# Kernel optimization log

Measured on AMD Instinct MI355X. Metric: run time of the kernel, lower is better.

The kernel has to match this reference:

```python
import jax, jax.numpy as jnp
import numpy as np

N, E, IN, H, OUT = 100000, 1200000, 128, 64, 2
L = 3          # num GCN layers
EPS = 1e-5     # BatchNorm eps


def setup_inputs() -> dict:
    key = jax.random.key(0)
    ks = jax.random.split(key, 14)
    x = jax.random.normal(ks[0], (N, IN), dtype=jnp.float32)
    edge_index = jax.random.randint(ks[1], (2, E), 0, N, dtype=jnp.int64)
    # GCNConv weights (glorot-ish scale) and biases
    w0 = jax.random.normal(ks[2], (IN, H), dtype=jnp.float32) / np.float32(np.sqrt(IN))
    w1 = jax.random.normal(ks[3], (H, H), dtype=jnp.float32) / np.float32(np.sqrt(H))
    w2 = jax.random.normal(ks[4], (H, H), dtype=jnp.float32) / np.float32(np.sqrt(H))
    biases = jax.random.normal(ks[5], (L, H), dtype=jnp.float32) * 0.01
    # BatchNorm (eval mode): gamma, beta, running mean/var per layer
    gamma = jnp.ones((L, H), jnp.float32) + 0.1 * jax.random.normal(ks[6], (L, H), dtype=jnp.float32)
    beta = 0.1 * jax.random.normal(ks[7], (L, H), dtype=jnp.float32)
    run_mean = 0.1 * jax.random.normal(ks[8], (L, H), dtype=jnp.float32)
    run_var = 0.5 + jax.random.uniform(ks[9], (L, H), dtype=jnp.float32)  # strictly positive
    # classifier
    cls_w = jax.random.normal(ks[10], (H, OUT), dtype=jnp.float32) / np.float32(np.sqrt(H))
    cls_b = jnp.zeros((OUT,), jnp.float32)
    return {"x": x, "edge_index": edge_index, "w0": w0, "w1": w1, "w2": w2,
            "biases": biases, "gamma": gamma, "beta": beta,
            "run_mean": run_mean, "run_var": run_var,
            "cls_w": cls_w, "cls_b": cls_b}


def reference(x, edge_index, w0, w1, w2, biases, gamma, beta, run_mean, run_var, cls_w, cls_b):
    n = x.shape[0]
    loop = jnp.arange(n, dtype=edge_index.dtype)
    row = jnp.concatenate([edge_index[0], loop])  # source (with self-loops)
    col = jnp.concatenate([edge_index[1], loop])  # target (with self-loops)
    # symmetric normalization: D^{-1/2} (A+I) D^{-1/2}, degree on target index
    deg = jax.ops.segment_sum(jnp.ones(row.shape, x.dtype), col, num_segments=n)
    dinv = jnp.where(deg > 0, jax.lax.rsqrt(deg), 0.0)
    norm = dinv[row] * dinv[col]  # [E+N]

    h = x
    for l, w in enumerate((w0, w1, w2)):
        h = h @ w                                                   # [N,H]
        msg = norm[:, None] * h[row]                                # gather + scale [E+N,H]
        h = jax.ops.segment_sum(msg, col, num_segments=n) + biases[l]
        # BatchNorm1d (eval) + ReLU
        scale = gamma[l] * jax.lax.rsqrt(run_var[l] + EPS)
        h = jax.nn.relu((h - run_mean[l]) * scale + beta[l])
        # dropout is identity in eval mode
    return h @ cls_w + cls_b  # [N, OUT]
```

## Files before the change

kernel.cpp:

```cpp
#include <hip/hip_runtime.h>
#include <hip/hip_fp16.h>

#define EPS 1e-5f
#define ABITS 9
#define ACHUNK 4096
#define BCAP 8192
#define BCSR 12288
#define CSHIFT 13
#define NCHUNK 16

typedef _Float16 half8 __attribute__((ext_vector_type(8)));
typedef float floatx4 __attribute__((ext_vector_type(4)));


__global__ __launch_bounds__(256) void bucketA_kernel(const int* __restrict__ ei, int E,
                                                      int* __restrict__ bucket_fill, unsigned* __restrict__ tmp) {
    __shared__ int2 edg[ACHUNK];
    __shared__ int hist[256], lbase[256], lcur[256];
    int t = threadIdx.x;
    hist[t] = 0; lcur[t] = 0;
    __syncthreads();
    int e0 = blockIdx.x * ACHUNK;
    int e1 = e0 + ACHUNK; if (e1 > E) e1 = E;
    int ne = e1 - e0;
    for (int idx = t; idx < ne; idx += 256) {
        int r = ei[e0 + idx], c = ei[E + e0 + idx];
        edg[idx] = make_int2(r, c);
        atomicAdd(&hist[c >> ABITS], 1);
    }
    __syncthreads();
    int h = hist[t];
    if (h) lbase[t] = atomicAdd(&bucket_fill[t], h);
    __syncthreads();
    for (int idx = t; idx < ne; idx += 256) {
        int2 e = edg[idx];
        int b = e.y >> ABITS;
        int l = atomicAdd(&lcur[b], 1);
        tmp[(size_t)b * BCAP + lbase[b] + l] = ((unsigned)(e.y & 511) << 17) | (unsigned)e.x;
    }
}

__global__ __launch_bounds__(256) void bucketB_kernel(const unsigned* __restrict__ tmp,
                                                      const int* __restrict__ bucket_fill,
                                                      int2* __restrict__ rowse, float* __restrict__ dinv,
                                                      int* __restrict__ csr, int* __restrict__ perm, int n) {
    __shared__ unsigned edg[BCAP];
    __shared__ int cnt2[512 * NCHUNK];
    __shared__ int ps[256];
    __shared__ int ccnt[16], cbaseS[16];
    int b = blockIdx.x, t = threadIdx.x;
    int n0 = b << ABITS;
    int cntN = n - n0; if (cntN > 512) cntN = 512;
    int ne = bucket_fill[b]; if (ne > BCAP) ne = BCAP;
    int base = b * BCAP;
    int cbase = b * BCSR;
    if (t < 16) ccnt[t] = 0;
    for (int i = t; i < 512 * NCHUNK; i += 256) cnt2[i] = 0;
    for (int idx = t; idx < ne; idx += 256) edg[idx] = tmp[(size_t)base + idx];
    __syncthreads();
    for (int idx = t; idx < ne; idx += 256) {
        unsigned e = edg[idx];
        int dstOff = e >> 17, src = e & 0x1FFFF;
        atomicAdd(&cnt2[dstOff * NCHUNK + (src >> CSHIFT)], 1);
    }
    __syncthreads();
    int c0 = 0, c1 = 0;
#pragma unroll
    for (int c = 0; c < NCHUNK; ++c) {
        c0 += cnt2[(2 * t) * NCHUNK + c];
        c1 += cnt2[(2 * t + 1) * NCHUNK + c];
    }
    int k0c = (c0 + 7) >> 3; if (k0c > 15) k0c = 15;
    int k1c = (c1 + 7) >> 3; if (k1c > 15) k1c = 15;
    int rank0 = 0, rank1 = 0;
    if (2 * t < cntN)     rank0 = atomicAdd(&ccnt[k0c], 1);
    if (2 * t + 1 < cntN) rank1 = atomicAdd(&ccnt[k1c], 1);
    int p0 = (c0 + 7) & ~7, p1 = (c1 + 7) & ~7;
    int s = p0 + p1;
    ps[t] = s;
    __syncthreads();
    for (int off = 1; off < 256; off <<= 1) {
        int u = (t >= off) ? ps[t - off] : 0;
        __syncthreads();
        ps[t] += u;
        __syncthreads();
    }
    int excl = ps[t] - s;
    int st0 = cbase + excl, st1 = cbase + excl + p0;
    if (2 * t < cntN) {
        rowse[n0 + 2 * t] = make_int2(st0, st0 + c0);
        dinv[n0 + 2 * t] = rsqrtf((float)(c0 + 1));
    }
    if (2 * t + 1 < cntN) {
        rowse[n0 + 2 * t + 1] = make_int2(st1, st1 + c1);
        dinv[n0 + 2 * t + 1] = rsqrtf((float)(c1 + 1));
    }
    if (2 * t < cntN)
        for (int j = c0; j < p0; ++j) csr[st0 + j] = n0 + 2 * t;
    if (2 * t + 1 < cntN)
        for (int j = c1; j < p1; ++j) csr[st1 + j] = n0 + 2 * t + 1;
    int run = st0;
#pragma unroll
    for (int c = 0; c < NCHUNK; ++c) {
        int v = cnt2[(2 * t) * NCHUNK + c];
        cnt2[(2 * t) * NCHUNK + c] = run;
        run += v;
    }
    run = st1;
#pragma unroll
    for (int c = 0; c < NCHUNK; ++c) {
        int v = cnt2[(2 * t + 1) * NCHUNK + c];
        cnt2[(2 * t + 1) * NCHUNK + c] = run;
        run += v;
    }
    if (t < 16) {
        int sacc = 0;
        for (int j = 0; j < t; ++j) sacc += ccnt[j];
        cbaseS[t] = sacc;
    }
    __syncthreads();
    if (2 * t < cntN)     perm[n0 + cbaseS[k0c] + rank0] = n0 + 2 * t;
    if (2 * t + 1 < cntN) perm[n0 + cbaseS[k1c] + rank1] = n0 + 2 * t + 1;
    for (int idx = t; idx < ne; idx += 256) {
        unsigned e = edg[idx];
        int dstOff = e >> 17, src = e & 0x1FFFF;
        int key = dstOff * NCHUNK + (src >> CSHIFT);
        int pos = atomicAdd(&cnt2[key], 1);
        csr[pos] = src;
    }
}


template <int K, typename TIN>
__global__ __launch_bounds__(256) void gemm_kernel(const TIN* __restrict__ A, const float* __restrict__ W,
                                                   const float* __restrict__ dinv, __half* __restrict__ out, int n) {
    const int KP = K + 8;
    __shared__ _Float16 Ah[64 * (K + 8)];
    __shared__ _Float16 Wt[64 * (K + 8)];
    int tid = threadIdx.x;

    for (int idx = tid; idx < K * 64; idx += 256) {
        int k = idx >> 6, c = idx & 63;
        Wt[c * KP + k] = (_Float16)W[idx];
    }
    int row0 = blockIdx.x * 64;
    const TIN* Ab = A + (size_t)row0 * K;
    int limit = (n - row0) * K; if (limit > 64 * K) limit = 64 * K;

    if constexpr (sizeof(TIN) == 4) {
        for (int f = tid * 4; f < 64 * K; f += 1024) {
            float4 v = make_float4(0.f, 0.f, 0.f, 0.f);
            if (f + 3 < limit) {
                v = *(const float4*)((const float*)Ab + f);
            } else {
                if (f + 0 < limit) v.x = ((const float*)Ab)[f + 0];
                if (f + 1 < limit) v.y = ((const float*)Ab)[f + 1];
                if (f + 2 < limit) v.z = ((const float*)Ab)[f + 2];
            }
            int row = f / K, k = f % K;
            _Float16* dst = Ah + row * KP + k;
            dst[0] = (_Float16)v.x; dst[1] = (_Float16)v.y;
            dst[2] = (_Float16)v.z; dst[3] = (_Float16)v.w;
        }
    } else {
        for (int f = tid * 8; f < 64 * K; f += 2048) {
            uint4 v = make_uint4(0, 0, 0, 0);
            if (f + 7 < limit) {
                v = *(const uint4*)((const __half*)Ab + f);
            } else {
                const __half* hp = (const __half*)Ab;
                __half tmp8[8];
                for (int j = 0; j < 8; ++j) tmp8[j] = (f + j < limit) ? hp[f + j] : __half(0);
                v = *(const uint4*)tmp8;
            }
            int row = f / K, k = f % K;
            *(uint4*)(Ah + row * KP + k) = v;
        }
    }
    __syncthreads();

    int w = tid >> 6, lane = tid & 63;
    int m = lane & 15, quad = lane >> 4;
    const _Float16* Aw = Ah + (size_t)(w * 16 + m) * KP + quad * 8;
    const _Float16* Bw = Wt + (size_t)m * KP + quad * 8;

    floatx4 acc0 = {0.f, 0.f, 0.f, 0.f}, acc1 = acc0, acc2 = acc0, acc3 = acc0;
    for (int k0 = 0; k0 < K; k0 += 32) {
        half8 a  = *(const half8*)(Aw + k0);
        half8 b0 = *(const half8*)(Bw + 0 * 16 * KP + k0);
        half8 b1 = *(const half8*)(Bw + 1 * 16 * KP + k0);
        half8 b2 = *(const half8*)(Bw + 2 * 16 * KP + k0);
        half8 b3 = *(const half8*)(Bw + 3 * 16 * KP + k0);
        acc0 = __builtin_amdgcn_mfma_f32_16x16x32_f16(a, b0, acc0, 0, 0, 0);
        acc1 = __builtin_amdgcn_mfma_f32_16x16x32_f16(a, b1, acc1, 0, 0, 0);
        acc2 = __builtin_amdgcn_mfma_f32_16x16x32_f16(a, b2, acc2, 0, 0, 0);
        acc3 = __builtin_amdgcn_mfma_f32_16x16x32_f16(a, b3, acc3, 0, 0, 0);
    }

    int rbase = row0 + w * 16 + quad * 4;
#pragma unroll
    for (int r = 0; r < 4; ++r) {
        int row = rbase + r;
        if (row < n) {
            float dv = dinv[row];
            __half* o = out + (size_t)row * 64 + m;
            o[0]  = __float2half(acc0[r] * dv);
            o[16] = __float2half(acc1[r] * dv);
            o[32] = __float2half(acc2[r] * dv);
            o[48] = __float2half(acc3[r] * dv);
        }
    }
}


__device__ __forceinline__ void agg_add8(float4& lo, float4& hi, uint4 raw) {
    float2 p0 = __half22float2(*(const __half2*)&raw.x);
    float2 p1 = __half22float2(*(const __half2*)&raw.y);
    float2 p2 = __half22float2(*(const __half2*)&raw.z);
    float2 p3 = __half22float2(*(const __half2*)&raw.w);
    lo.x += p0.x; lo.y += p0.y; lo.z += p1.x; lo.w += p1.y;
    hi.x += p2.x; hi.y += p2.y; hi.z += p3.x; hi.w += p3.y;
}

__device__ __forceinline__ void agg_core(const __half* __restrict__ t, const float* __restrict__ dinv,
                                         const int2* __restrict__ rowse, const int* __restrict__ csr,
                                         const float* __restrict__ bias, const float* __restrict__ gamma,
                                         const float* __restrict__ beta, const float* __restrict__ mean,
                                         const float* __restrict__ var,
                                         int i, int fl, float4& resL, float4& resH, float& di) {
    uint4 self = *(const uint4*)(t + (size_t)i * 64 + fl * 8);

    float4 lo = make_float4(0.f, 0.f, 0.f, 0.f);
    float4 hi = make_float4(0.f, 0.f, 0.f, 0.f);

    int2 se = rowse[i];
    int deg = se.y - se.x;
    int padEnd = se.x + ((deg + 7) & ~7);
    for (int e = se.x; e < padEnd; e += 8) {
        int s0 = csr[e + 0], s1 = csr[e + 1], s2 = csr[e + 2], s3 = csr[e + 3];
        int s4 = csr[e + 4], s5 = csr[e + 5], s6 = csr[e + 6], s7 = csr[e + 7];
        uint4 r0 = *(const uint4*)(t + (size_t)s0 * 64 + fl * 8);
        uint4 r1 = *(const uint4*)(t + (size_t)s1 * 64 + fl * 8);
        uint4 r2 = *(const uint4*)(t + (size_t)s2 * 64 + fl * 8);
        uint4 r3 = *(const uint4*)(t + (size_t)s3 * 64 + fl * 8);
        uint4 r4 = *(const uint4*)(t + (size_t)s4 * 64 + fl * 8);
        uint4 r5 = *(const uint4*)(t + (size_t)s5 * 64 + fl * 8);
        uint4 r6 = *(const uint4*)(t + (size_t)s6 * 64 + fl * 8);
        uint4 r7 = *(const uint4*)(t + (size_t)s7 * 64 + fl * 8);
        agg_add8(lo, hi, r0); agg_add8(lo, hi, r1); agg_add8(lo, hi, r2); agg_add8(lo, hi, r3);
        agg_add8(lo, hi, r4); agg_add8(lo, hi, r5); agg_add8(lo, hi, r6); agg_add8(lo, hi, r7);
    }

    float coef = 1.0f - (float)(padEnd - se.y);
    {
        float2 p0 = __half22float2(*(const __half2*)&self.x);
        float2 p1 = __half22float2(*(const __half2*)&self.y);
        float2 p2 = __half22float2(*(const __half2*)&self.z);
        float2 p3 = __half22float2(*(const __half2*)&self.w);
        lo.x += coef * p0.x; lo.y += coef * p0.y; lo.z += coef * p1.x; lo.w += coef * p1.y;
        hi.x += coef * p2.x; hi.y += coef * p2.y; hi.z += coef * p3.x; hi.w += coef * p3.y;
    }

    di = dinv[i];
    lo.x *= di; lo.y *= di; lo.z *= di; lo.w *= di;
    hi.x *= di; hi.y *= di; hi.z *= di; hi.w *= di;

    float4 bbL = ((const float4*)bias)[2 * fl],  bbH = ((const float4*)bias)[2 * fl + 1];
    float4 ggL = ((const float4*)gamma)[2 * fl], ggH = ((const float4*)gamma)[2 * fl + 1];
    float4 beL = ((const float4*)beta)[2 * fl],  beH = ((const float4*)beta)[2 * fl + 1];
    float4 mmL = ((const float4*)mean)[2 * fl],  mmH = ((const float4*)mean)[2 * fl + 1];
    float4 vvL = ((const float4*)var)[2 * fl],   vvH = ((const float4*)var)[2 * fl + 1];
    resL.x = fmaxf((lo.x + bbL.x - mmL.x) * (ggL.x * rsqrtf(vvL.x + EPS)) + beL.x, 0.f);
    resL.y = fmaxf((lo.y + bbL.y - mmL.y) * (ggL.y * rsqrtf(vvL.y + EPS)) + beL.y, 0.f);
    resL.z = fmaxf((lo.z + bbL.z - mmL.z) * (ggL.z * rsqrtf(vvL.z + EPS)) + beL.z, 0.f);
    resL.w = fmaxf((lo.w + bbL.w - mmL.w) * (ggL.w * rsqrtf(vvL.w + EPS)) + beL.w, 0.f);
    resH.x = fmaxf((hi.x + bbH.x - mmH.x) * (ggH.x * rsqrtf(vvH.x + EPS)) + beH.x, 0.f);
    resH.y = fmaxf((hi.y + bbH.y - mmH.y) * (ggH.y * rsqrtf(vvH.y + EPS)) + beH.y, 0.f);
    resH.z = fmaxf((hi.z + bbH.z - mmH.z) * (ggH.z * rsqrtf(vvH.z + EPS)) + beH.z, 0.f);
    resH.w = fmaxf((hi.w + bbH.w - mmH.w) * (ggH.w * rsqrtf(vvH.w + EPS)) + beH.w, 0.f);
}

__global__ __launch_bounds__(256, 4) void agg_gemm_kernel(
        const __half* __restrict__ t, const float* __restrict__ dinv,
        const int2* __restrict__ rowse, const int* __restrict__ csr,
        const int* __restrict__ perm,
        const float* __restrict__ bias, const float* __restrict__ gamma,
        const float* __restrict__ beta, const float* __restrict__ mean,
        const float* __restrict__ var,
        const float* __restrict__ W,
        __half* __restrict__ tout, int n) {
    const int KP = 72;
    __shared__ _Float16 Ah[32 * 72];
    __shared__ _Float16 Wt[64 * 72];
    __shared__ int   nidS[32];
    __shared__ float dvS[32];

    int tid = threadIdx.x;
    for (int idx = tid; idx < 64 * 64; idx += 256) {
        int k = idx >> 6, c = idx & 63;
        Wt[c * KP + k] = (_Float16)W[idx];
    }

    int wave = tid >> 6, lane = tid & 63;
    int g = lane >> 3, fl = lane & 7;
    int slotInBlk = wave * 8 + g;
    int slot = blockIdx.x * 32 + slotInBlk;
    bool act = slot < n;

    if (act) {
        int i = perm[slot];
        float4 resL, resH; float di;
        agg_core(t, dinv, rowse, csr, bias, gamma, beta, mean, var, i, fl, resL, resH, di);
        __half2 h0 = __floats2half2_rn(resL.x, resL.y);
        __half2 h1 = __floats2half2_rn(resL.z, resL.w);
        __half2 h2 = __floats2half2_rn(resH.x, resH.y);
        __half2 h3 = __floats2half2_rn(resH.z, resH.w);
        uint4 pk;
        pk.x = *(unsigned*)&h0; pk.y = *(unsigned*)&h1;
        pk.z = *(unsigned*)&h2; pk.w = *(unsigned*)&h3;
        *(uint4*)(Ah + slotInBlk * KP + fl * 8) = pk;
        if (fl == 0) { nidS[slotInBlk] = i; dvS[slotInBlk] = di; }
    } else {
        uint4 z = make_uint4(0, 0, 0, 0);
        *(uint4*)(Ah + slotInBlk * KP + fl * 8) = z;
        if (fl == 0) { nidS[slotInBlk] = 0; dvS[slotInBlk] = 0.f; }
    }
    __syncthreads();

    int m = lane & 15, quad = lane >> 4;
    int mrow = (wave & 1) * 16;
    int c0 = (wave >> 1) * 32;
    const _Float16* Aw = Ah + (mrow + m) * KP + quad * 8;
    const _Float16* Bw = Wt + (c0 + m) * KP + quad * 8;

    floatx4 acc0 = {0.f, 0.f, 0.f, 0.f}, acc1 = acc0;
#pragma unroll
    for (int k0 = 0; k0 < 64; k0 += 32) {
        half8 a  = *(const half8*)(Aw + k0);
        half8 b0 = *(const half8*)(Bw + k0);
        half8 b1 = *(const half8*)(Bw + 16 * KP + k0);
        acc0 = __builtin_amdgcn_mfma_f32_16x16x32_f16(a, b0, acc0, 0, 0, 0);
        acc1 = __builtin_amdgcn_mfma_f32_16x16x32_f16(a, b1, acc1, 0, 0, 0);
    }
    __syncthreads();

#pragma unroll
    for (int r = 0; r < 4; ++r) {
        int row = mrow + quad * 4 + r;
        float dv = dvS[row];
        Ah[row * KP + c0 + m]      = (_Float16)(acc0[r] * dv);
        Ah[row * KP + c0 + 16 + m] = (_Float16)(acc1[r] * dv);
    }
    __syncthreads();

    if (act) {
        int node = nidS[slotInBlk];
        uint4 v = *(const uint4*)(Ah + slotInBlk * KP + fl * 8);
        *(uint4*)(tout + (size_t)node * 64 + fl * 8) = v;
    }
}

__global__ __launch_bounds__(256, 4) void agg_cls_kernel(
        const __half* __restrict__ t, const float* __restrict__ dinv,
        const int2* __restrict__ rowse, const int* __restrict__ csr,
        const int* __restrict__ perm,
        const float* __restrict__ bias, const float* __restrict__ gamma,
        const float* __restrict__ beta, const float* __restrict__ mean,
        const float* __restrict__ var,
        float* __restrict__ fout,
        const float* __restrict__ cls_w, const float* __restrict__ cls_b,
        int n) {
    int wave = threadIdx.x >> 6;
    int lane = threadIdx.x & 63;
    int g = lane >> 3;
    int fl = lane & 7;
    int slot = (blockIdx.x * (blockDim.x >> 6) + wave) * 8 + g;
    if (slot >= n) return;
    int i = perm[slot];

    float4 resL, resH; float di;
    agg_core(t, dinv, rowse, csr, bias, gamma, beta, mean, var, i, fl, resL, resH, di);

    const float4* cw = (const float4*)cls_w;
    float4 cwA = cw[4 * fl + 0], cwB = cw[4 * fl + 1], cwC = cw[4 * fl + 2], cwD = cw[4 * fl + 3];
    float c0 = resL.x * cwA.x + resL.y * cwA.z + resL.z * cwB.x + resL.w * cwB.z
             + resH.x * cwC.x + resH.y * cwC.z + resH.z * cwD.x + resH.w * cwD.z;
    float c1 = resL.x * cwA.y + resL.y * cwA.w + resL.z * cwB.y + resL.w * cwB.w
             + resH.x * cwC.y + resH.y * cwC.w + resH.z * cwD.y + resH.w * cwD.w;
    for (int off = 4; off > 0; off >>= 1) {
        c0 += __shfl_xor(c0, off);
        c1 += __shfl_xor(c1, off);
    }
    if (fl == 0) {
        fout[(size_t)i * 2 + 0] = c0 + cls_b[0];
        fout[(size_t)i * 2 + 1] = c1 + cls_b[1];
    }
}


extern "C" void kernel_launch(void* const* d_in, const int* in_sizes, int n_in,
                              void* d_out, int out_size, void* d_ws, size_t ws_size,
                              hipStream_t stream) {
    const float* x      = (const float*)d_in[0];
    const int*   ei     = (const int*)d_in[1];
    const float* w0     = (const float*)d_in[2];
    const float* w1     = (const float*)d_in[3];
    const float* w2     = (const float*)d_in[4];
    const float* biases = (const float*)d_in[5];
    const float* gamma  = (const float*)d_in[6];
    const float* beta   = (const float*)d_in[7];
    const float* rmean  = (const float*)d_in[8];
    const float* rvar   = (const float*)d_in[9];
    const float* cls_w  = (const float*)d_in[10];
    const float* cls_b  = (const float*)d_in[11];
    float* out = (float*)d_out;

    const int IN = 128, H = 64;
    const int N = in_sizes[0] / IN;
    const int E = in_sizes[1] / 2;

    char* p = (char*)d_ws;
    auto carve = [&](size_t bytes) { void* q = (void*)p; p += (bytes + 255) & ~(size_t)255; return q; };
    float* dinv    = (float*)carve((size_t)N * 4);
    int2*  rowse   = (int2*)carve((size_t)N * 8);
    int*   bucket_fill = (int*)carve((size_t)256 * 4);
    int*   perm    = (int*)carve((size_t)N * 4);
    unsigned* tmp  = (unsigned*)carve((size_t)256 * BCAP * 4);
    int*   csr     = (int*)carve((size_t)256 * BCSR * 4);
    __half* tA     = (__half*)carve((size_t)N * H * 2);
    __half* tB     = (__half*)carve((size_t)N * H * 2);

    int nbuckets = (N + (1 << ABITS) - 1) >> ABITS;
    int na = (E + ACHUNK - 1) / ACHUNK;

    hipMemsetAsync(bucket_fill, 0, (size_t)256 * 4, stream);
    bucketA_kernel<<<na, 256, 0, stream>>>(ei, E, bucket_fill, tmp);
    bucketB_kernel<<<nbuckets, 256, 0, stream>>>(tmp, bucket_fill, rowse, dinv, csr, perm, N);

    int gemm_grid = (N + 63) / 64;
    int agg_grid  = (N + 31) / 32;

    gemm_kernel<128, float><<<gemm_grid, 256, 0, stream>>>(x, w0, dinv, tA, N);
    agg_gemm_kernel<<<agg_grid, 256, 0, stream>>>(tA, dinv, rowse, csr, perm,
        biases + 0, gamma + 0, beta + 0, rmean + 0, rvar + 0, w1, tB, N);
    agg_gemm_kernel<<<agg_grid, 256, 0, stream>>>(tB, dinv, rowse, csr, perm,
        biases + H, gamma + H, beta + H, rmean + H, rvar + H, w2, tA, N);
    agg_cls_kernel<<<agg_grid, 256, 0, stream>>>(tA, dinv, rowse, csr, perm,
        biases + 2 * H, gamma + 2 * H, beta + 2 * H, rmean + 2 * H, rvar + 2 * H,
        out, cls_w, cls_b, N);
}
```

Baseline: 251.5 us.

## Halve CSR bucket size to double bucketB parallelism and use wave-shuffle scan

Bucket granularity drops from 512 to 256 destination nodes, so the CSR build kernel launches about twice as many blocks (around 391 instead of 196) with smaller shared-memory footprints. Each thread now handles one node, and the block prefix sum uses wave-level shuffles plus a small cross-wave add in place of a barrier-heavy shared-memory scan. BucketA uses smaller edge chunks and loops over up to 512 bucket histogram entries, which adds more global atomics on bucket_fill. Per-bucket capacities are halved, so bucket overflow becomes more likely if the degree distribution is skewed.

```diff
diff --git a/kernel.cpp b/kernel.cpp
--- a/kernel.cpp
+++ b/kernel.cpp
@@ -2,10 +2,11 @@
 #include <hip/hip_fp16.h>
 
 #define EPS 1e-5f
-#define ABITS 9
-#define ACHUNK 4096
-#define BCAP 8192
-#define BCSR 12288
+#define ABITS 8
+#define NBKT_MAX 512
+#define ACHUNK 2048
+#define BCAP 4096
+#define BCSR 6144
 #define CSHIFT 13
 #define NCHUNK 16
 
@@ -16,9 +17,9 @@
 __global__ __launch_bounds__(256) void bucketA_kernel(const int* __restrict__ ei, int E,
                                                       int* __restrict__ bucket_fill, unsigned* __restrict__ tmp) {
     __shared__ int2 edg[ACHUNK];
-    __shared__ int hist[256], lbase[256], lcur[256];
+    __shared__ int hist[NBKT_MAX], lbase[NBKT_MAX], lcur[NBKT_MAX];
     int t = threadIdx.x;
-    hist[t] = 0; lcur[t] = 0;
+    for (int i = t; i < NBKT_MAX; i += 256) { hist[i] = 0; lcur[i] = 0; }
     __syncthreads();
     int e0 = blockIdx.x * ACHUNK;
     int e1 = e0 + ACHUNK; if (e1 > E) e1 = E;
@@ -29,14 +30,16 @@
         atomicAdd(&hist[c >> ABITS], 1);
     }
     __syncthreads();
-    int h = hist[t];
-    if (h) lbase[t] = atomicAdd(&bucket_fill[t], h);
+    for (int i = t; i < NBKT_MAX; i += 256) {
+        int h = hist[i];
+        if (h) lbase[i] = atomicAdd(&bucket_fill[i], h);
+    }
     __syncthreads();
     for (int idx = t; idx < ne; idx += 256) {
         int2 e = edg[idx];
         int b = e.y >> ABITS;
         int l = atomicAdd(&lcur[b], 1);
-        tmp[(size_t)b * BCAP + lbase[b] + l] = ((unsigned)(e.y & 511) << 17) | (unsigned)e.x;
+        tmp[(size_t)b * BCAP + lbase[b] + l] = ((unsigned)(e.y & 255) << 17) | (unsigned)e.x;
     }
 }
 
@@ -45,17 +48,18 @@
                                                       int2* __restrict__ rowse, float* __restrict__ dinv,
                                                       int* __restrict__ csr, int* __restrict__ perm, int n) {
     __shared__ unsigned edg[BCAP];
-    __shared__ int cnt2[512 * NCHUNK];
-    __shared__ int ps[256];
+    __shared__ int cnt2[256 * NCHUNK];
+    __shared__ int wsum[4];
     __shared__ int ccnt[16], cbaseS[16];
     int b = blockIdx.x, t = threadIdx.x;
+    int lane = t & 63, wv = t >> 6;
     int n0 = b << ABITS;
-    int cntN = n - n0; if (cntN > 512) cntN = 512;
+    int cntN = n - n0; if (cntN > 256) cntN = 256;
     int ne = bucket_fill[b]; if (ne > BCAP) ne = BCAP;
     int base = b * BCAP;
     int cbase = b * BCSR;
     if (t < 16) ccnt[t] = 0;
-    for (int i = t; i < 512 * NCHUNK; i += 256) cnt2[i] = 0;
+    for (int i = t; i < 256 * NCHUNK; i += 256) cnt2[i] = 0;
     for (int idx = t; idx < ne; idx += 256) edg[idx] = tmp[(size_t)base + idx];
     __syncthreads();
     for (int idx = t; idx < ne; idx += 256) {
@@ -64,54 +68,36 @@
         atomicAdd(&cnt2[dstOff * NCHUNK + (src >> CSHIFT)], 1);
     }
     __syncthreads();
-    int c0 = 0, c1 = 0;
+    int c0 = 0;
+#pragma unroll
+    for (int c = 0; c < NCHUNK; ++c) c0 += cnt2[t * NCHUNK + c];
+    int k0c = (c0 + 7) >> 3; if (k0c > 15) k0c = 15;
+    int rank0 = 0;
+    if (t < cntN) rank0 = atomicAdd(&ccnt[k0c], 1);
+    int p0 = (c0 + 7) & ~7;
+    int v = p0;
+#pragma unroll
+    for (int off = 1; off < 64; off <<= 1) {
+        int u = __shfl_up(v, off);
+        if (lane >= off) v += u;
+    }
+    if (lane == 63) wsum[wv] = v;
+    __syncthreads();
+    int addv = 0;
+    for (int j = 0; j < wv; ++j) addv += wsum[j];
+    int excl = v + addv - p0;
+    int st0 = cbase + excl;
+    if (t < cntN) {
+        rowse[n0 + t] = make_int2(st0, st0 + c0);
+        dinv[n0 + t] = rsqrtf((float)(c0 + 1));
+        for (int j = c0; j < p0; ++j) csr[st0 + j] = n0 + t;
+    }
+    int run = st0;
 #pragma unroll
     for (int c = 0; c < NCHUNK; ++c) {
-        c0 += cnt2[(2 * t) * NCHUNK + c];
-        c1 += cnt2[(2 * t + 1) * NCHUNK + c];
-    }
-    int k0c = (c0 + 7) >> 3; if (k0c > 15) k0c = 15;
-    int k1c = (c1 + 7) >> 3; if (k1c > 15) k1c = 15;
-    int rank0 = 0, rank1 = 0;
-    if (2 * t < cntN)     rank0 = atomicAdd(&ccnt[k0c], 1);
-    if (2 * t + 1 < cntN) rank1 = atomicAdd(&ccnt[k1c], 1);
-    int p0 = (c0 + 7) & ~7, p1 = (c1 + 7) & ~7;
-    int s = p0 + p1;
-    ps[t] = s;
-    __syncthreads();
-    for (int off = 1; off < 256; off <<= 1) {
-        int u = (t >= off) ? ps[t - off] : 0;
-        __syncthreads();
-        ps[t] += u;
-        __syncthreads();
-    }
-    int excl = ps[t] - s;
-    int st0 = cbase + excl, st1 = cbase + excl + p0;
-    if (2 * t < cntN) {
-        rowse[n0 + 2 * t] = make_int2(st0, st0 + c0);
-        dinv[n0 + 2 * t] = rsqrtf((float)(c0 + 1));
-    }
-    if (2 * t + 1 < cntN) {
-        rowse[n0 + 2 * t + 1] = make_int2(st1, st1 + c1);
-        dinv[n0 + 2 * t + 1] = rsqrtf((float)(c1 + 1));
-    }
-    if (2 * t < cntN)
-        for (int j = c0; j < p0; ++j) csr[st0 + j] = n0 + 2 * t;
-    if (2 * t + 1 < cntN)
-        for (int j = c1; j < p1; ++j) csr[st1 + j] = n0 + 2 * t + 1;
-    int run = st0;
-#pragma unroll
-    for (int c = 0; c < NCHUNK; ++c) {
-        int v = cnt2[(2 * t) * NCHUNK + c];
-        cnt2[(2 * t) * NCHUNK + c] = run;
-        run += v;
-    }
-    run = st1;
-#pragma unroll
-    for (int c = 0; c < NCHUNK; ++c) {
-        int v = cnt2[(2 * t + 1) * NCHUNK + c];
-        cnt2[(2 * t + 1) * NCHUNK + c] = run;
-        run += v;
+        int vv = cnt2[t * NCHUNK + c];
+        cnt2[t * NCHUNK + c] = run;
+        run += vv;
     }
     if (t < 16) {
         int sacc = 0;
@@ -119,8 +105,7 @@
         cbaseS[t] = sacc;
     }
     __syncthreads();
-    if (2 * t < cntN)     perm[n0 + cbaseS[k0c] + rank0] = n0 + 2 * t;
-    if (2 * t + 1 < cntN) perm[n0 + cbaseS[k1c] + rank1] = n0 + 2 * t + 1;
+    if (t < cntN) perm[n0 + cbaseS[k0c] + rank0] = n0 + t;
     for (int idx = t; idx < ne; idx += 256) {
         unsigned e = edg[idx];
         int dstOff = e >> 17, src = e & 0x1FFFF;
@@ -423,17 +408,17 @@
     auto carve = [&](size_t bytes) { void* q = (void*)p; p += (bytes + 255) & ~(size_t)255; return q; };
     float* dinv    = (float*)carve((size_t)N * 4);
     int2*  rowse   = (int2*)carve((size_t)N * 8);
-    int*   bucket_fill = (int*)carve((size_t)256 * 4);
+    int*   bucket_fill = (int*)carve((size_t)NBKT_MAX * 4);
     int*   perm    = (int*)carve((size_t)N * 4);
-    unsigned* tmp  = (unsigned*)carve((size_t)256 * BCAP * 4);
-    int*   csr     = (int*)carve((size_t)256 * BCSR * 4);
+    unsigned* tmp  = (unsigned*)carve((size_t)NBKT_MAX * BCAP * 4);
+    int*   csr     = (int*)carve((size_t)NBKT_MAX * BCSR * 4);
     __half* tA     = (__half*)carve((size_t)N * H * 2);
     __half* tB     = (__half*)carve((size_t)N * H * 2);
 
     int nbuckets = (N + (1 << ABITS) - 1) >> ABITS;
     int na = (E + ACHUNK - 1) / ACHUNK;
 
-    hipMemsetAsync(bucket_fill, 0, (size_t)256 * 4, stream);
+    hipMemsetAsync(bucket_fill, 0, (size_t)NBKT_MAX * 4, stream);
     bucketA_kernel<<<na, 256, 0, stream>>>(ei, E, bucket_fill, tmp);
     bucketB_kernel<<<nbuckets, 256, 0, stream>>>(tmp, bucket_fill, rowse, dinv, csr, perm, N);
 
```

New measurement: 250.3 us. About the same (-0.5%).
